# Kernel optimization log

Measured on AMD Instinct MI355X. Metric: run time of the kernel, lower is better.

Reference implementation:

```python
import jax, jax.numpy as jnp
import numpy as np

B, LX, LM, D = 4, 512, 512, 256

def setup_inputs() -> dict:
    key = jax.random.key(0)
    ks = jax.random.split(key, 7)
    s = 1.0 / np.sqrt(D)
    return {
        "x": jax.random.normal(ks[0], (B, LX, D), jnp.float32),
        "memory": jax.random.normal(ks[1], (B, LM, D), jnp.float32),
        "memory_mask": jax.random.randint(ks[2], (B, LM), 0, 2, jnp.int32),
        "W1": jax.random.normal(ks[3], (D, D), jnp.float32) * s,
        "b1": jax.random.normal(ks[4], (D,), jnp.float32) * s,
        "W2": jax.random.normal(ks[5], (D, D), jnp.float32) * s,
        "Wt": jax.random.normal(ks[6], (D,), jnp.float32) * s,
    }

def reference(x, memory, memory_mask, W1, b1, W2, Wt):
    # item1: (B, Lx, D); item2: (B, Lm, D)
    item1 = jnp.einsum("bxd,ed->bxe", x, W1) + b1
    item2 = jnp.einsum("bmd,ed->bme", memory, W2)
    # additive attention: tanh of broadcast sum, then reduce D to scalar logit
    item = item1[:, :, None, :] + item2[:, None, :, :]  # (B, Lx, Lm, D)
    S_logit = jnp.einsum("bxmd,d->bxm", jnp.tanh(item), Wt)
    S_logit = jnp.where(memory_mask[:, None, :] == 0, jnp.float32(-10000.0), S_logit)
    return S_logit
```

## Files before the change

### kernel.cpp

```cpp
#include <hip/hip_runtime.h>

namespace {

constexpr int B = 4, LX = 512, LM = 512, D = 256;
constexpr float KSCALE = 2.8853900817779268f;
constexpr float CLAMP = 15.0f;

typedef __attribute__((ext_vector_type(8))) short short8;
typedef __attribute__((ext_vector_type(4))) float f32x4;

__device__ __forceinline__ unsigned bfbits(float f) {
    unsigned u = __float_as_uint(f);
    u += 0x7FFFu + ((u >> 16) & 1u);
    return u >> 16;
}
__device__ __forceinline__ int pack2(float a, float b) {
    return (int)(bfbits(a) | (bfbits(b) << 16));
}

__global__ __launch_bounds__(256) void proj_mfma(
    const float* __restrict__ x, const float* __restrict__ mem,
    const float* __restrict__ W1, const float* __restrict__ b1v,
    const float* __restrict__ W2, float* __restrict__ E1, float* __restrict__ E2)
{
    const int tid = threadIdx.x;
    const int m0c = blockIdx.x * 32;
    const int e0  = blockIdx.y * 64;
    const int z   = m0c >= 2048;
    const int r0  = z ? (m0c - 2048) : m0c;
    const float* __restrict__ A = (z ? mem : x) + (size_t)r0 * D;
    const float* __restrict__ W = z ? W2 : W1;
    float* __restrict__ E = z ? E2 : E1;

    __shared__ short sA[32][40];
    __shared__ short sW[64][40];

    const int wv = tid >> 6, lane = tid & 63;
    const int lr = lane & 15, quad = lane >> 4;
    const int g   = wv & 1;
    const int cg0 = (wv >> 1) * 2;

    const int srA = tid >> 3;
    const int scA = (tid & 7) * 4;

    f32x4 acc0 = {0.f, 0.f, 0.f, 0.f};
    f32x4 acc1 = {0.f, 0.f, 0.f, 0.f};

    for (int kc = 0; kc < D; kc += 32) {
        float4 av = *(const float4*)&A[(size_t)srA * D + kc + scA];
        float4 w0 = *(const float4*)&W[(size_t)(e0 + srA) * D + kc + scA];
        float4 w1 = *(const float4*)&W[(size_t)(e0 + 32 + srA) * D + kc + scA];
        __syncthreads();
        *(int2*)&sA[srA][scA]      = make_int2(pack2(av.x, av.y), pack2(av.z, av.w));
        *(int2*)&sW[srA][scA]      = make_int2(pack2(w0.x, w0.y), pack2(w0.z, w0.w));
        *(int2*)&sW[srA + 32][scA] = make_int2(pack2(w1.x, w1.y), pack2(w1.z, w1.w));
        __syncthreads();
        short8 af  = *(const short8*)&sA[g * 16 + lr][quad * 8];
        short8 bf0 = *(const short8*)&sW[cg0 * 16 + lr][quad * 8];
        short8 bf1 = *(const short8*)&sW[cg0 * 16 + 16 + lr][quad * 8];
        acc0 = __builtin_amdgcn_mfma_f32_16x16x32_bf16(af, bf0, acc0, 0, 0, 0);
        acc1 = __builtin_amdgcn_mfma_f32_16x16x32_bf16(af, bf1, acc1, 0, 0, 0);
    }

    const float bias0 = z ? 0.f : b1v[e0 + cg0 * 16 + lr];
    const float bias1 = z ? 0.f : b1v[e0 + cg0 * 16 + 16 + lr];
#pragma unroll
    for (int reg = 0; reg < 4; ++reg) {
        const int row = r0 + g * 16 + quad * 4 + reg;
        float a0 = KSCALE * (acc0[reg] + bias0);
        float a1 = KSCALE * (acc1[reg] + bias1);
        a0 = fminf(fmaxf(a0, -CLAMP), CLAMP);
        a1 = fminf(fmaxf(a1, -CLAMP), CLAMP);
        E[(size_t)row * D + e0 + cg0 * 16 + lr]      = __builtin_amdgcn_exp2f(a0);
        E[(size_t)row * D + e0 + cg0 * 16 + 16 + lr] = __builtin_amdgcn_exp2f(a1);
    }
}

__global__ __launch_bounds__(256) void tanh_score_kernel(
    const float* __restrict__ e1p, const float* __restrict__ e2p,
    const float* __restrict__ Wt, const int* __restrict__ mask,
    float* __restrict__ out)
{
    const int tid = threadIdx.x;
    const int b  = blockIdx.z;
    const int x0 = blockIdx.y * 32;
    const int m0 = blockIdx.x * 64;

    __shared__ float sA[32][68];
    __shared__ float sB[64][68];

    const int tx = tid & 15, ty = tid >> 4;
    const int rA = tid >> 3, cA = (tid & 7) * 8;
    const int rB = tid >> 2, cB = (tid & 3) * 16;

    float a00 = 0.f, a01 = 0.f, a02 = 0.f, a03 = 0.f;
    float a10 = 0.f, a11 = 0.f, a12 = 0.f, a13 = 0.f;
    float accW = 0.f;

    for (int c = 0; c < 4; ++c) {
        const int dB = c * 64;
        const float* gA = &e1p[((size_t)b * LX + x0 + rA) * D + dB + cA];
        const float* gB = &e2p[((size_t)b * LM + m0 + rB) * D + dB + cB];
        float4 A0 = *(const float4*)(gA + 0);
        float4 A1 = *(const float4*)(gA + 4);
        float4 B0 = *(const float4*)(gB + 0);
        float4 B1 = *(const float4*)(gB + 4);
        float4 B2 = *(const float4*)(gB + 8);
        float4 B3 = *(const float4*)(gB + 12);
        __syncthreads();
        *(float4*)&sA[rA][cA + 0] = A0;
        *(float4*)&sA[rA][cA + 4] = A1;
        *(float4*)&sB[rB][cB + 0]  = B0;
        *(float4*)&sB[rB][cB + 4]  = B1;
        *(float4*)&sB[rB][cB + 8]  = B2;
        *(float4*)&sB[rB][cB + 12] = B3;
        __syncthreads();

#pragma unroll 4
        for (int d = 0; d < 64; d += 4) {
            const float4 wq  = *(const float4*)&Wt[dB + d];
            const float4 ra0 = *(const float4*)&sA[ty][d];
            const float4 ra1 = *(const float4*)&sA[ty + 16][d];
            const float4 rb0 = *(const float4*)&sB[tx][d];
            const float4 rb1 = *(const float4*)&sB[tx + 16][d];
            const float4 rb2 = *(const float4*)&sB[tx + 32][d];
            const float4 rb3 = *(const float4*)&sB[tx + 48][d];
            accW += (wq.x + wq.y) + (wq.z + wq.w);

#define QUAD(ra, rb, accv) {                                           \
            const float A0_ = fmaf((ra).x, (rb).x, 1.f);               \
            const float A1_ = fmaf((ra).y, (rb).y, 1.f);               \
            const float A2_ = fmaf((ra).z, (rb).z, 1.f);               \
            const float A3_ = fmaf((ra).w, (rb).w, 1.f);               \
            const float L_ = A0_ * A1_, R_ = A2_ * A3_;                \
            const float den_ = L_ * R_;                                \
            const float t0_ = fmaf(wq.y, A0_, wq.x * A1_);             \
            const float t1_ = fmaf(wq.w, A2_, wq.z * A3_);             \
            const float N_ = fmaf(t1_, L_, t0_ * R_);                  \
            (accv) = fmaf(N_, __builtin_amdgcn_rcpf(den_), (accv)); }

            QUAD(ra0, rb0, a00); QUAD(ra0, rb1, a01);
            QUAD(ra0, rb2, a02); QUAD(ra0, rb3, a03);
            QUAD(ra1, rb0, a10); QUAD(ra1, rb1, a11);
            QUAD(ra1, rb2, a12); QUAD(ra1, rb3, a13);
#undef QUAD
        }
    }

    const int xA = x0 + ty, xB = x0 + ty + 16;
    const int mm[4] = {m0 + tx, m0 + tx + 16, m0 + tx + 32, m0 + tx + 48};
    float s0[4] = {accW - 2.f * a00, accW - 2.f * a01,
                   accW - 2.f * a02, accW - 2.f * a03};
    float s1[4] = {accW - 2.f * a10, accW - 2.f * a11,
                   accW - 2.f * a12, accW - 2.f * a13};
#pragma unroll
    for (int k = 0; k < 4; ++k) {
        const bool keep = mask[b * LM + mm[k]] != 0;
        out[((size_t)b * LX + xA) * LM + mm[k]] = keep ? s0[k] : -10000.f;
        out[((size_t)b * LX + xB) * LM + mm[k]] = keep ? s1[k] : -10000.f;
    }
}

}

extern "C" void kernel_launch(void* const* d_in, const int* in_sizes, int n_in,
                              void* d_out, int out_size, void* d_ws, size_t ws_size,
                              hipStream_t stream)
{
    const float* x    = (const float*)d_in[0];
    const float* mem  = (const float*)d_in[1];
    const int*   mask = (const int*)d_in[2];
    const float* W1   = (const float*)d_in[3];
    const float* b1   = (const float*)d_in[4];
    const float* W2   = (const float*)d_in[5];
    const float* Wt   = (const float*)d_in[6];
    float* out = (float*)d_out;

    float* E1 = (float*)d_ws;
    float* E2 = E1 + (size_t)B * LX * D;

    proj_mfma<<<dim3(128, 4), 256, 0, stream>>>(x, mem, W1, b1, W2, E1, E2);

    tanh_score_kernel<<<dim3(LM / 64, LX / 32, B), 256, 0, stream>>>(
        E1, E2, Wt, mask, out);
}
```

Baseline: 104.8 us.

## Compact unmasked memory columns and skip tanh scoring for masked positions

A new prep kernel fills the whole output with -10000, compacts the unmasked memory indices of each batch into an index list via ballot/popcount, and precomputes the sum of Wt. The score kernel then gathers only unmasked memory rows, returns early for tiles past the valid count, and scatters results to the original columns. About half of the tanh work is skipped for the random mask, at the cost of an extra launch, a full output fill, and scattered writes. Precomputing the Wt sum also removes a per-iteration reduction from the inner loop.

```diff
diff --git a/kernel.cpp b/kernel.cpp
--- a/kernel.cpp
+++ b/kernel.cpp
@@ -16,6 +16,39 @@
 }
 __device__ __forceinline__ int pack2(float a, float b) {
     return (int)(bfbits(a) | (bfbits(b) << 16));
+}
+
+__global__ __launch_bounds__(256) void prep_fill(
+    const int* __restrict__ mask, const float* __restrict__ Wt,
+    float* __restrict__ out, unsigned short* __restrict__ midx,
+    int* __restrict__ cnt, float* __restrict__ sumWt)
+{
+    const int tid = threadIdx.x;
+    float4* o4 = (float4*)out;
+    o4[(size_t)blockIdx.x * 256 + tid] =
+        make_float4(-10000.f, -10000.f, -10000.f, -10000.f);
+
+    if (blockIdx.x == 0) {
+        const int w = tid >> 6, lane = tid & 63;
+        const unsigned long long lmask = (1ULL << lane) - 1ULL;
+        int basec = 0;
+#pragma unroll
+        for (int k = 0; k < 8; ++k) {
+            const int i = k * 64 + lane;
+            const int mv = mask[w * LM + i];
+            const unsigned long long bal = __ballot(mv != 0);
+            const int pos = basec + (int)__popcll(bal & lmask);
+            if (mv) midx[w * LM + pos] = (unsigned short)i;
+            basec += (int)__popcll(bal);
+        }
+        for (int j = basec + lane; j < LM; j += 64) midx[w * LM + j] = 0;
+        if (lane == 0) cnt[w] = basec;
+    } else if (blockIdx.x == 1 && tid < 64) {
+        float v = Wt[tid] + Wt[tid + 64] + Wt[tid + 128] + Wt[tid + 192];
+#pragma unroll
+        for (int off = 32; off; off >>= 1) v += __shfl_xor(v, off);
+        if (tid == 0) *sumWt = v;
+    }
 }
 
 __global__ __launch_bounds__(256) void proj_mfma(
@@ -39,7 +72,6 @@
     const int lr = lane & 15, quad = lane >> 4;
     const int g   = wv & 1;
     const int cg0 = (wv >> 1) * 2;
-
     const int srA = tid >> 3;
     const int scA = (tid & 7) * 4;
 
@@ -78,13 +110,16 @@
 
 __global__ __launch_bounds__(256) void tanh_score_kernel(
     const float* __restrict__ e1p, const float* __restrict__ e2p,
-    const float* __restrict__ Wt, const int* __restrict__ mask,
+    const float* __restrict__ Wt, const unsigned short* __restrict__ midx,
+    const int* __restrict__ cnt, const float* __restrict__ sumWt,
     float* __restrict__ out)
 {
     const int tid = threadIdx.x;
-    const int b  = blockIdx.z;
-    const int x0 = blockIdx.y * 32;
-    const int m0 = blockIdx.x * 64;
+    const int x0 = blockIdx.x * 32;
+    const int b  = blockIdx.y;
+    const int j0 = blockIdx.z * 64;
+    const int Nb = cnt[b];
+    if (j0 >= Nb) return;
 
     __shared__ float sA[32][68];
     __shared__ float sB[64][68];
@@ -92,21 +127,22 @@
     const int tx = tid & 15, ty = tid >> 4;
     const int rA = tid >> 3, cA = (tid & 7) * 8;
     const int rB = tid >> 2, cB = (tid & 3) * 16;
+    const int growB = midx[b * LM + j0 + rB];
+
+    const float* gAbase = &e1p[((size_t)b * LX + x0 + rA) * D + cA];
+    const float* gBbase = &e2p[((size_t)b * LM + growB) * D + cB];
 
     float a00 = 0.f, a01 = 0.f, a02 = 0.f, a03 = 0.f;
     float a10 = 0.f, a11 = 0.f, a12 = 0.f, a13 = 0.f;
-    float accW = 0.f;
 
     for (int c = 0; c < 4; ++c) {
         const int dB = c * 64;
-        const float* gA = &e1p[((size_t)b * LX + x0 + rA) * D + dB + cA];
-        const float* gB = &e2p[((size_t)b * LM + m0 + rB) * D + dB + cB];
-        float4 A0 = *(const float4*)(gA + 0);
-        float4 A1 = *(const float4*)(gA + 4);
-        float4 B0 = *(const float4*)(gB + 0);
-        float4 B1 = *(const float4*)(gB + 4);
-        float4 B2 = *(const float4*)(gB + 8);
-        float4 B3 = *(const float4*)(gB + 12);
+        float4 A0 = *(const float4*)(gAbase + dB + 0);
+        float4 A1 = *(const float4*)(gAbase + dB + 4);
+        float4 B0 = *(const float4*)(gBbase + dB + 0);
+        float4 B1 = *(const float4*)(gBbase + dB + 4);
+        float4 B2 = *(const float4*)(gBbase + dB + 8);
+        float4 B3 = *(const float4*)(gBbase + dB + 12);
         __syncthreads();
         *(float4*)&sA[rA][cA + 0] = A0;
         *(float4*)&sA[rA][cA + 4] = A1;
@@ -125,7 +161,6 @@
             const float4 rb1 = *(const float4*)&sB[tx + 16][d];
             const float4 rb2 = *(const float4*)&sB[tx + 32][d];
             const float4 rb3 = *(const float4*)&sB[tx + 48][d];
-            accW += (wq.x + wq.y) + (wq.z + wq.w);
 
 #define QUAD(ra, rb, accv) {                                           \
             const float A0_ = fmaf((ra).x, (rb).x, 1.f);               \
@@ -147,17 +182,20 @@
         }
     }
 
+    const float sW = *sumWt;
     const int xA = x0 + ty, xB = x0 + ty + 16;
-    const int mm[4] = {m0 + tx, m0 + tx + 16, m0 + tx + 32, m0 + tx + 48};
-    float s0[4] = {accW - 2.f * a00, accW - 2.f * a01,
-                   accW - 2.f * a02, accW - 2.f * a03};
-    float s1[4] = {accW - 2.f * a10, accW - 2.f * a11,
-                   accW - 2.f * a12, accW - 2.f * a13};
+    const float s0[4] = {sW - 2.f * a00, sW - 2.f * a01,
+                         sW - 2.f * a02, sW - 2.f * a03};
+    const float s1[4] = {sW - 2.f * a10, sW - 2.f * a11,
+                         sW - 2.f * a12, sW - 2.f * a13};
 #pragma unroll
     for (int k = 0; k < 4; ++k) {
-        const bool keep = mask[b * LM + mm[k]] != 0;
-        out[((size_t)b * LX + xA) * LM + mm[k]] = keep ? s0[k] : -10000.f;
-        out[((size_t)b * LX + xB) * LM + mm[k]] = keep ? s1[k] : -10000.f;
+        const int j = j0 + tx + 16 * k;
+        if (j < Nb) {
+            const int m = midx[b * LM + j];
+            out[((size_t)b * LX + xA) * LM + m] = s0[k];
+            out[((size_t)b * LX + xB) * LM + m] = s1[k];
+        }
     }
 }
 
@@ -178,9 +216,14 @@
 
     float* E1 = (float*)d_ws;
     float* E2 = E1 + (size_t)B * LX * D;
+    unsigned short* midx = (unsigned short*)(E2 + (size_t)B * LM * D);
+    int* cnt = (int*)(midx + B * LM);
+    float* sumWt = (float*)(cnt + B);
+
+    prep_fill<<<dim3(1024), 256, 0, stream>>>(mask, Wt, out, midx, cnt, sumWt);
 
     proj_mfma<<<dim3(128, 4), 256, 0, stream>>>(x, mem, W1, b1, W2, E1, E2);
 
-    tanh_score_kernel<<<dim3(LM / 64, LX / 32, B), 256, 0, stream>>>(
-        E1, E2, Wt, mask, out);
-}
+    tanh_score_kernel<<<dim3(LX / 32, B, LM / 64), 256, 0, stream>>>(
+        E1, E2, Wt, midx, cnt, sumWt, out);
+}
```

Result: no change. 106.5 us (+1.6%).

## Store exp projections as paired bf16 and use packed f32x2 math in score kernel

Applied to the files above, without the earlier changes.

The projection kernel now writes exp-scaled activations as bf16, interleaving rows r and r+16 into one 32-bit word. The score kernel unpacks each word into an f32x2 and runs the rational tanh-sum on packed two-wide FMAs over 8 dimensions per reciprocal, using swapped pairs to cover the cross terms. This halves intermediate memory traffic and LDS footprint and aims to double ALU throughput via packed FP32 ops, while amortising the reciprocal over more terms. It costs precision through bf16 storage, and the clamp drops from 15 to 7.5, presumably to keep the product of 8 terms from overflowing.

```diff
diff --git a/kernel.cpp b/kernel.cpp
--- a/kernel.cpp
+++ b/kernel.cpp
@@ -4,10 +4,11 @@
 
 constexpr int B = 4, LX = 512, LM = 512, D = 256;
 constexpr float KSCALE = 2.8853900817779268f;
-constexpr float CLAMP = 15.0f;
+constexpr float CLAMP = 7.5f;
 
 typedef __attribute__((ext_vector_type(8))) short short8;
 typedef __attribute__((ext_vector_type(4))) float f32x4;
+typedef __attribute__((ext_vector_type(2))) float f32x2;
 
 __device__ __forceinline__ unsigned bfbits(float f) {
     unsigned u = __float_as_uint(f);
@@ -17,11 +18,18 @@
 __device__ __forceinline__ int pack2(float a, float b) {
     return (int)(bfbits(a) | (bfbits(b) << 16));
 }
+__device__ __forceinline__ f32x2 up2(unsigned u) {
+    f32x2 r;
+    r.x = __uint_as_float(u << 16);
+    r.y = __uint_as_float(u & 0xFFFF0000u);
+    return r;
+}
 
 __global__ __launch_bounds__(256) void proj_mfma(
     const float* __restrict__ x, const float* __restrict__ mem,
     const float* __restrict__ W1, const float* __restrict__ b1v,
-    const float* __restrict__ W2, float* __restrict__ E1, float* __restrict__ E2)
+    const float* __restrict__ W2,
+    unsigned short* __restrict__ E1h, unsigned short* __restrict__ E2h)
 {
     const int tid = threadIdx.x;
     const int m0c = blockIdx.x * 32;
@@ -30,7 +38,7 @@
     const int r0  = z ? (m0c - 2048) : m0c;
     const float* __restrict__ A = (z ? mem : x) + (size_t)r0 * D;
     const float* __restrict__ W = z ? W2 : W1;
-    float* __restrict__ E = z ? E2 : E1;
+    unsigned short* __restrict__ Eh = z ? E2h : E1h;
 
     __shared__ short sA[32][40];
     __shared__ short sW[64][40];
@@ -39,7 +47,6 @@
     const int lr = lane & 15, quad = lane >> 4;
     const int g   = wv & 1;
     const int cg0 = (wv >> 1) * 2;
-
     const int srA = tid >> 3;
     const int scA = (tid & 7) * 4;
 
@@ -64,20 +71,24 @@
 
     const float bias0 = z ? 0.f : b1v[e0 + cg0 * 16 + lr];
     const float bias1 = z ? 0.f : b1v[e0 + cg0 * 16 + 16 + lr];
+    const int ec0 = e0 + cg0 * 16 + lr;
 #pragma unroll
     for (int reg = 0; reg < 4; ++reg) {
-        const int row = r0 + g * 16 + quad * 4 + reg;
+        const int pair = quad * 4 + reg;
+        const size_t base = (size_t)((r0 >> 5) * 16 + pair) * 256;
         float a0 = KSCALE * (acc0[reg] + bias0);
         float a1 = KSCALE * (acc1[reg] + bias1);
         a0 = fminf(fmaxf(a0, -CLAMP), CLAMP);
         a1 = fminf(fmaxf(a1, -CLAMP), CLAMP);
-        E[(size_t)row * D + e0 + cg0 * 16 + lr]      = __builtin_amdgcn_exp2f(a0);
-        E[(size_t)row * D + e0 + cg0 * 16 + 16 + lr] = __builtin_amdgcn_exp2f(a1);
+        Eh[(base + ec0) * 2 + g] =
+            (unsigned short)bfbits(__builtin_amdgcn_exp2f(a0));
+        Eh[(base + ec0 + 16) * 2 + g] =
+            (unsigned short)bfbits(__builtin_amdgcn_exp2f(a1));
     }
 }
 
 __global__ __launch_bounds__(256) void tanh_score_kernel(
-    const float* __restrict__ e1p, const float* __restrict__ e2p,
+    const unsigned* __restrict__ E1p, const unsigned* __restrict__ E2p,
     const float* __restrict__ Wt, const int* __restrict__ mask,
     float* __restrict__ out)
 {
@@ -85,79 +96,114 @@
     const int b  = blockIdx.z;
     const int x0 = blockIdx.y * 32;
     const int m0 = blockIdx.x * 64;
-
-    __shared__ float sA[32][68];
-    __shared__ float sB[64][68];
+    const int xt = (b * LX + x0) >> 5;
+    const int mt = (b * LM + m0) >> 5;
+
+    __shared__ unsigned sA[16 * 132];
+    __shared__ unsigned sB[32 * 132];
 
     const int tx = tid & 15, ty = tid >> 4;
-    const int rA = tid >> 3, cA = (tid & 7) * 8;
-    const int rB = tid >> 2, cB = (tid & 3) * 16;
-
-    float a00 = 0.f, a01 = 0.f, a02 = 0.f, a03 = 0.f;
-    float a10 = 0.f, a11 = 0.f, a12 = 0.f, a13 = 0.f;
-    float accW = 0.f;
-
-    for (int c = 0; c < 4; ++c) {
-        const int dB = c * 64;
-        const float* gA = &e1p[((size_t)b * LX + x0 + rA) * D + dB + cA];
-        const float* gB = &e2p[((size_t)b * LM + m0 + rB) * D + dB + cB];
-        float4 A0 = *(const float4*)(gA + 0);
-        float4 A1 = *(const float4*)(gA + 4);
-        float4 B0 = *(const float4*)(gB + 0);
-        float4 B1 = *(const float4*)(gB + 4);
-        float4 B2 = *(const float4*)(gB + 8);
-        float4 B3 = *(const float4*)(gB + 12);
-        __syncthreads();
-        *(float4*)&sA[rA][cA + 0] = A0;
-        *(float4*)&sA[rA][cA + 4] = A1;
-        *(float4*)&sB[rB][cB + 0]  = B0;
-        *(float4*)&sB[rB][cB + 4]  = B1;
-        *(float4*)&sB[rB][cB + 8]  = B2;
-        *(float4*)&sB[rB][cB + 12] = B3;
-        __syncthreads();
-
-#pragma unroll 4
-        for (int d = 0; d < 64; d += 4) {
-            const float4 wq  = *(const float4*)&Wt[dB + d];
-            const float4 ra0 = *(const float4*)&sA[ty][d];
-            const float4 ra1 = *(const float4*)&sA[ty + 16][d];
-            const float4 rb0 = *(const float4*)&sB[tx][d];
-            const float4 rb1 = *(const float4*)&sB[tx + 16][d];
-            const float4 rb2 = *(const float4*)&sB[tx + 32][d];
-            const float4 rb3 = *(const float4*)&sB[tx + 48][d];
-            accW += (wq.x + wq.y) + (wq.z + wq.w);
-
-#define QUAD(ra, rb, accv) {                                           \
-            const float A0_ = fmaf((ra).x, (rb).x, 1.f);               \
-            const float A1_ = fmaf((ra).y, (rb).y, 1.f);               \
-            const float A2_ = fmaf((ra).z, (rb).z, 1.f);               \
-            const float A3_ = fmaf((ra).w, (rb).w, 1.f);               \
-            const float L_ = A0_ * A1_, R_ = A2_ * A3_;                \
-            const float den_ = L_ * R_;                                \
-            const float t0_ = fmaf(wq.y, A0_, wq.x * A1_);             \
-            const float t1_ = fmaf(wq.w, A2_, wq.z * A3_);             \
-            const float N_ = fmaf(t1_, L_, t0_ * R_);                  \
-            (accv) = fmaf(N_, __builtin_amdgcn_rcpf(den_), (accv)); }
-
-            QUAD(ra0, rb0, a00); QUAD(ra0, rb1, a01);
-            QUAD(ra0, rb2, a02); QUAD(ra0, rb3, a03);
-            QUAD(ra1, rb0, a10); QUAD(ra1, rb1, a11);
-            QUAD(ra1, rb2, a12); QUAD(ra1, rb3, a13);
-#undef QUAD
+    const int pA = tid >> 4, cA = (tid & 15) * 4;
+    const int rB = tid >> 3, cB = (tid & 7) * 4;
+    const unsigned* gA = E1p + (size_t)(xt * 16 + pA) * 256;
+    const unsigned* gB = E2p + (size_t)((mt + (rB >> 4)) * 16 + (rB & 15)) * 256;
+
+    float sumW = 0.f;
+#pragma unroll
+    for (int i = 0; i < 256; i += 4) {
+        const float4 w = *(const float4*)&Wt[i];
+        sumW += (w.x + w.y) + (w.z + w.w);
+    }
+
+    f32x2 acc01s = {0.f, 0.f}, acc01w = {0.f, 0.f};
+    f32x2 acc23s = {0.f, 0.f}, acc23w = {0.f, 0.f};
+    const f32x2 one2 = {1.f, 1.f};
+
+    for (int c = 0; c < 2; ++c) {
+        const int dB = c * 128;
+        uint4 A0 = *(const uint4*)(gA + dB + cA);
+        uint4 A1 = *(const uint4*)(gA + dB + 64 + cA);
+        uint4 B0 = *(const uint4*)(gB + dB + cB);
+        uint4 B1 = *(const uint4*)(gB + dB + 32 + cB);
+        uint4 B2 = *(const uint4*)(gB + dB + 64 + cB);
+        uint4 B3 = *(const uint4*)(gB + dB + 96 + cB);
+        __syncthreads();
+        *(uint4*)&sA[pA * 132 + cA]      = A0;
+        *(uint4*)&sA[pA * 132 + 64 + cA] = A1;
+        *(uint4*)&sB[rB * 132 + cB]      = B0;
+        *(uint4*)&sB[rB * 132 + 32 + cB] = B1;
+        *(uint4*)&sB[rB * 132 + 64 + cB] = B2;
+        *(uint4*)&sB[rB * 132 + 96 + cB] = B3;
+        __syncthreads();
+
+#pragma unroll 1
+        for (int d = 0; d < 128; d += 8) {
+            const uint4 ua0 = *(const uint4*)&sA[ty * 132 + d];
+            const uint4 ua1 = *(const uint4*)&sA[ty * 132 + d + 4];
+            const uint4 ub0 = *(const uint4*)&sB[tx * 132 + d];
+            const uint4 ub1 = *(const uint4*)&sB[tx * 132 + d + 4];
+            const uint4 uc0 = *(const uint4*)&sB[(16 + tx) * 132 + d];
+            const uint4 uc1 = *(const uint4*)&sB[(16 + tx) * 132 + d + 4];
+            const float4 w0 = *(const float4*)&Wt[dB + d];
+            const float4 w1 = *(const float4*)&Wt[dB + d + 4];
+
+            const f32x2 a_[8] = {up2(ua0.x), up2(ua0.y), up2(ua0.z), up2(ua0.w),
+                                 up2(ua1.x), up2(ua1.y), up2(ua1.z), up2(ua1.w)};
+            const f32x2 p_[8] = {up2(ub0.x), up2(ub0.y), up2(ub0.z), up2(ub0.w),
+                                 up2(ub1.x), up2(ub1.y), up2(ub1.z), up2(ub1.w)};
+            const f32x2 q_[8] = {up2(uc0.x), up2(uc0.y), up2(uc0.z), up2(uc0.w),
+                                 up2(uc1.x), up2(uc1.y), up2(uc1.z), up2(uc1.w)};
+            const float wv[8] = {w0.x, w0.y, w0.z, w0.w, w1.x, w1.y, w1.z, w1.w};
+
+#define SPL(s)  ((f32x2){(s), (s)})
+#define FMA2(A_, B_, C_) __builtin_elementwise_fma((A_), (B_), (C_))
+#define OCT(BX, accv) { \
+    const f32x2 T0 = FMA2(a_[0], BX(0), one2), T1 = FMA2(a_[1], BX(1), one2); \
+    const f32x2 T2 = FMA2(a_[2], BX(2), one2), T3 = FMA2(a_[3], BX(3), one2); \
+    const f32x2 T4 = FMA2(a_[4], BX(4), one2), T5 = FMA2(a_[5], BX(5), one2); \
+    const f32x2 T6 = FMA2(a_[6], BX(6), one2), T7 = FMA2(a_[7], BX(7), one2); \
+    const f32x2 L0 = T0 * T1, L1 = T2 * T3, L2 = T4 * T5, L3 = T6 * T7;       \
+    const f32x2 Q0 = L0 * L1, Q1 = L2 * L3;                                   \
+    const f32x2 den = Q0 * Q1;                                                \
+    const f32x2 n0 = FMA2(SPL(wv[0]), T1, SPL(wv[1]) * T0);                   \
+    const f32x2 n1 = FMA2(SPL(wv[2]), T3, SPL(wv[3]) * T2);                   \
+    const f32x2 n2 = FMA2(SPL(wv[4]), T5, SPL(wv[5]) * T4);                   \
+    const f32x2 n3 = FMA2(SPL(wv[6]), T7, SPL(wv[7]) * T6);                   \
+    const f32x2 u0 = FMA2(n0, L1, n1 * L0), u1 = FMA2(n2, L3, n3 * L2);       \
+    const f32x2 N  = FMA2(u0, Q1, u1 * Q0);                                   \
+    f32x2 r; r.x = __builtin_amdgcn_rcpf(den.x);                              \
+             r.y = __builtin_amdgcn_rcpf(den.y);                              \
+    (accv) = FMA2(N, r, (accv)); }
+
+#define BP(i)  (p_[i])
+#define BPS(i) (__builtin_shufflevector(p_[i], p_[i], 1, 0))
+#define BQ(i)  (q_[i])
+#define BQS(i) (__builtin_shufflevector(q_[i], q_[i], 1, 0))
+            OCT(BP,  acc01s)
+            OCT(BPS, acc01w)
+            OCT(BQ,  acc23s)
+            OCT(BQS, acc23w)
+#undef BP
+#undef BPS
+#undef BQ
+#undef BQS
+#undef OCT
+#undef FMA2
+#undef SPL
         }
     }
 
-    const int xA = x0 + ty, xB = x0 + ty + 16;
-    const int mm[4] = {m0 + tx, m0 + tx + 16, m0 + tx + 32, m0 + tx + 48};
-    float s0[4] = {accW - 2.f * a00, accW - 2.f * a01,
-                   accW - 2.f * a02, accW - 2.f * a03};
-    float s1[4] = {accW - 2.f * a10, accW - 2.f * a11,
-                   accW - 2.f * a12, accW - 2.f * a13};
+    const int xA = x0 + ty, xB = x0 + 16 + ty;
+    const int mmv[4] = {m0 + tx, m0 + 16 + tx, m0 + 32 + tx, m0 + 48 + tx};
+    const float vA[4] = {acc01s.x, acc01w.x, acc23s.x, acc23w.x};
+    const float vB[4] = {acc01w.y, acc01s.y, acc23w.y, acc23s.y};
 #pragma unroll
     for (int k = 0; k < 4; ++k) {
-        const bool keep = mask[b * LM + mm[k]] != 0;
-        out[((size_t)b * LX + xA) * LM + mm[k]] = keep ? s0[k] : -10000.f;
-        out[((size_t)b * LX + xB) * LM + mm[k]] = keep ? s1[k] : -10000.f;
+        const bool keep = mask[b * LM + mmv[k]] != 0;
+        out[((size_t)b * LX + xA) * LM + mmv[k]] =
+            keep ? (sumW - 2.f * vA[k]) : -10000.f;
+        out[((size_t)b * LX + xB) * LM + mmv[k]] =
+            keep ? (sumW - 2.f * vB[k]) : -10000.f;
     }
 }
 
@@ -176,11 +222,12 @@
     const float* Wt   = (const float*)d_in[6];
     float* out = (float*)d_out;
 
-    float* E1 = (float*)d_ws;
-    float* E2 = E1 + (size_t)B * LX * D;
-
-    proj_mfma<<<dim3(128, 4), 256, 0, stream>>>(x, mem, W1, b1, W2, E1, E2);
+    unsigned* E1p = (unsigned*)d_ws;
+    unsigned* E2p = E1p + (size_t)(B * LX / 32) * 16 * 256;
+
+    proj_mfma<<<dim3(128, 4), 256, 0, stream>>>(
+        x, mem, W1, b1, W2, (unsigned short*)E1p, (unsigned short*)E2p);
 
     tanh_score_kernel<<<dim3(LM / 64, LX / 32, B), 256, 0, stream>>>(
-        E1, E2, Wt, mask, out);
-}
+        E1p, E2p, Wt, mask, out);
+}
```

Result: no change. 104.5 us (-0.3%).
